# Kernel tuning notes

Hardware: AMD Instinct MI355X
Metric: run time of the kernel (lower is better)

The kernel has to match this reference:

```python
import jax, jax.numpy as jnp
import numpy as np

N_HEAD = 16

def setup_inputs() -> dict:
    key = jax.random.key(0)
    k1, k2, k3 = jax.random.split(key, 3)
    B, T, C = 2, 2048, 1024
    x_norm_for_qk = jax.random.normal(k1, (B, T, C), dtype=jnp.float32)
    xt_current_for_v = jax.random.normal(k2, (B, T, C), dtype=jnp.float32)
    W_attn = jax.random.normal(k3, (C, 2 * C), dtype=jnp.float32) * (1.0 / np.sqrt(C))
    b_attn = jnp.zeros((2 * C,), dtype=jnp.float32)
    return {"x_norm_for_qk": x_norm_for_qk, "xt_current_for_v": xt_current_for_v,
            "W_attn": W_attn, "b_attn": b_attn}

def reference(x_norm_for_qk, xt_current_for_v, W_attn, b_attn):
    B, T, C = x_norm_for_qk.shape
    H = N_HEAD
    D = C // H  # head dim
    qk = x_norm_for_qk @ W_attn + b_attn          # [B,T,2C]
    q, k = qk[..., :C], qk[..., C:]
    q = q.reshape(B, T, H, D).transpose(0, 2, 1, 3)   # [B,H,T,D]
    k = k.reshape(B, T, H, D).transpose(0, 2, 1, 3)
    v = xt_current_for_v.reshape(B, T, H, D).transpose(0, 2, 1, 3)
    scale = 1.0 / np.sqrt(D).astype(np.float32)
    scores = jnp.einsum('bhqd,bhkd->bhqk', q, k) * scale  # [B,H,T,T]
    causal = jnp.tril(jnp.ones((T, T), dtype=bool))
    scores = jnp.where(causal[None, None], scores, jnp.float32(-jnp.inf))
    weights = jax.nn.softmax(scores, axis=-1)  # dropout p=0.0 -> identity
    y = jnp.einsum('bhqk,bhkd->bhqd', weights, v)
    return y.transpose(0, 2, 1, 3).reshape(B, T, C)
```

## Files before the change

kernel.cpp:

```cpp
#include <hip/hip_runtime.h>
#include <hip/hip_bf16.h>
#include <math.h>

typedef __attribute__((ext_vector_type(8))) short s8v;
typedef __attribute__((ext_vector_type(4))) float f4v;
typedef __attribute__((ext_vector_type(16))) float f16v;
typedef __attribute__((ext_vector_type(2))) unsigned int u32x2;
typedef unsigned short ush;
typedef unsigned int u32;

#define QSCALE 0.180336880f
#define FIXED_M 10.0f

static __device__ __forceinline__ ush f2bf(float f) {
    u32 x = __builtin_bit_cast(u32, f);
    return (ush)((x + 0x7fffu + ((x >> 16) & 1u)) >> 16);
}
static __device__ __forceinline__ u32 bfpack(float lo, float hi) {
    u32 a = __builtin_bit_cast(u32, lo) + 0x8000u;
    u32 b = __builtin_bit_cast(u32, hi) + 0x8000u;
    return __builtin_amdgcn_perm(b, a, 0x07060302);
}
static __device__ __forceinline__ u32 cvtpk(float lo, float hi) {
    u32 r;
    asm("v_cvt_pk_bf16_f32 %0, %1, %2" : "=v"(r) : "v"(lo), "v"(hi));
    return r;
}
static __device__ __forceinline__ void gl_lds16(const void* g, void* l) {
    __builtin_amdgcn_global_load_lds(
        (const __attribute__((address_space(1))) u32*)g,
        (__attribute__((address_space(3))) u32*)l, 16, 0, 0);
}
#if __has_builtin(__builtin_amdgcn_exp2f)
#define EXP2F(x) __builtin_amdgcn_exp2f(x)
#else
#define EXP2F(x) exp2f(x)
#endif

static __device__ __forceinline__ void pl32swap(u32& a, u32& b) {
#if __has_builtin(__builtin_amdgcn_permlane32_swap)
    u32x2 r = __builtin_amdgcn_permlane32_swap(a, b, false, false);
    a = r[0]; b = r[1];
#else
    asm volatile("v_permlane32_swap_b32 %0, %1" : "+v"(a), "+v"(b));
#endif
}
static __device__ __forceinline__ s8v mkfrag(u32 a, u32 b, u32 c, u32 d) {
    union { u32 w[4]; s8v v; } u;
    u.w[0] = a; u.w[1] = b; u.w[2] = c; u.w[3] = d;
    return u.v;
}

static __device__ __forceinline__ void softpack32(
    const f16v& s0, bool needmask, int kbase, int qg,
    float& lrp, s8v& pfa, s8v& pfb)
{
    float ps = 0.f;
    u32 w0[4], w1[4];
    if (needmask) {
        #pragma unroll
        for (int g4 = 0; g4 < 4; ++g4) {
            const int kb0 = kbase + 8 * g4;
            float e0a = (kb0 + 0 > qg) ? 0.f : EXP2F(s0[g4 * 4 + 0] - FIXED_M);
            float e0b = (kb0 + 1 > qg) ? 0.f : EXP2F(s0[g4 * 4 + 1] - FIXED_M);
            float e0c = (kb0 + 2 > qg) ? 0.f : EXP2F(s0[g4 * 4 + 2] - FIXED_M);
            float e0d = (kb0 + 3 > qg) ? 0.f : EXP2F(s0[g4 * 4 + 3] - FIXED_M);
            ps += (e0a + e0b) + (e0c + e0d);
            w0[g4] = cvtpk(e0a, e0b); w1[g4] = cvtpk(e0c, e0d);
        }
    } else {
        #pragma unroll
        for (int g4 = 0; g4 < 4; ++g4) {
            float e0a = EXP2F(s0[g4 * 4 + 0] - FIXED_M);
            float e0b = EXP2F(s0[g4 * 4 + 1] - FIXED_M);
            float e0c = EXP2F(s0[g4 * 4 + 2] - FIXED_M);
            float e0d = EXP2F(s0[g4 * 4 + 3] - FIXED_M);
            ps += (e0a + e0b) + (e0c + e0d);
            w0[g4] = cvtpk(e0a, e0b); w1[g4] = cvtpk(e0c, e0d);
        }
    }
    lrp += ps;
    pl32swap(w0[0], w0[1]); pl32swap(w1[0], w1[1]);
    pl32swap(w0[2], w0[3]); pl32swap(w1[2], w1[3]);
    pfa = mkfrag(w0[0], w1[0], w0[1], w1[1]);
    pfb = mkfrag(w0[2], w1[2], w0[3], w1[3]);
}

__global__ __launch_bounds__(256) void prep_kernel(
    const float* __restrict__ X, const float* __restrict__ W,
    const float* __restrict__ XV,
    ush* __restrict__ Xb, ush* __restrict__ Wt, ush* __restrict__ Vtb)
{
    __shared__ float Ts[64][68];
    const int tid = threadIdx.x;
    const int bid = blockIdx.x;
    if (bid < 2048) {
        const size_t i = ((size_t)bid * 256 + tid) * 8;
        float4 v0 = *(const float4*)(X + i);
        float4 v1 = *(const float4*)(X + i + 4);
        uint4 o;
        o.x = bfpack(v0.x, v0.y); o.y = bfpack(v0.z, v0.w);
        o.z = bfpack(v1.x, v1.y); o.w = bfpack(v1.z, v1.w);
        *(uint4*)(Xb + i) = o;
    } else if (bid < 2560) {
        const int id = bid - 2048;
        const int n0 = (id & 31) * 64, k0 = (id >> 5) * 64;
        #pragma unroll
        for (int p = 0; p < 4; ++p) {
            const int idx = p * 256 + tid;
            const int kr = idx >> 4, nc4 = idx & 15;
            float4 v = *(const float4*)(W + (size_t)(k0 + kr) * 2048 + n0 + nc4 * 4);
            Ts[kr][nc4 * 4 + 0] = v.x; Ts[kr][nc4 * 4 + 1] = v.y;
            Ts[kr][nc4 * 4 + 2] = v.z; Ts[kr][nc4 * 4 + 3] = v.w;
        }
        __syncthreads();
        const int n = tid >> 2, kb = (tid & 3) * 16;
        #pragma unroll
        for (int p = 0; p < 4; ++p) {
            const int k = kb + p * 4;
            ushort4 o;
            o.x = f2bf(Ts[k + 0][n]); o.y = f2bf(Ts[k + 1][n]);
            o.z = f2bf(Ts[k + 2][n]); o.w = f2bf(Ts[k + 3][n]);
            *(ushort4*)(Wt + (size_t)(n0 + n) * 1024 + k0 + k) = o;
        }
    } else {
        const int id = bid - 2560;
        const int t0 = (id & 31) * 64;
        const int bh = id >> 5;
        const int b = bh >> 4, h = bh & 15;
        #pragma unroll
        for (int p = 0; p < 4; ++p) {
            const int idx = p * 256 + tid;
            const int tr = idx >> 4, dc4 = idx & 15;
            float4 v = *(const float4*)(XV + (size_t)(b * 2048 + t0 + tr) * 1024
                                        + h * 64 + dc4 * 4);
            Ts[tr][dc4 * 4 + 0] = v.x; Ts[tr][dc4 * 4 + 1] = v.y;
            Ts[tr][dc4 * 4 + 2] = v.z; Ts[tr][dc4 * 4 + 3] = v.w;
        }
        __syncthreads();
        const int d = tid >> 2, tb = (tid & 3) * 16;
        #pragma unroll
        for (int p = 0; p < 4; ++p) {
            const int tq = tb + p * 4;
            ushort4 o;
            o.x = f2bf(Ts[tq + 0][d]); o.y = f2bf(Ts[tq + 1][d]);
            o.z = f2bf(Ts[tq + 2][d]); o.w = f2bf(Ts[tq + 3][d]);
            *(ushort4*)(Vtb + (size_t)((b * 16 + h) * 64 + d) * 2048 + t0 + tq) = o;
        }
    }
}

__global__ __launch_bounds__(256, 2) void gemm_kernel(
    const ush* __restrict__ Xb, const ush* __restrict__ Wt,
    const float* __restrict__ bias,
    ush* __restrict__ Qb, ush* __restrict__ Kb)
{
    __shared__ ush As[4][128 * 32];
    __shared__ ush Bs[4][128 * 32];

    const int tid = threadIdx.x;
    const int wid = tid >> 6, lane = tid & 63;
    const int quad = lane >> 4, l15 = lane & 15;
    const int wm = wid >> 1, wn = wid & 1;
    const int m0 = blockIdx.y * 128, n0 = blockIdx.x * 128;

    const int lrow = lane >> 2;
    const int lkk = (lane & 3) * 8;
    const size_t arow = (size_t)(m0 + wid * 32 + lrow);
    const size_t brow = (size_t)(n0 + wid * 32 + lrow);

    auto stage = [&](int k) {
        const int k0 = k * 32, sl = k & 3;
        gl_lds16(Xb + arow * 1024 + k0 + lkk, &As[sl][wid * 1024]);
        gl_lds16(Xb + (arow + 16) * 1024 + k0 + lkk, &As[sl][wid * 1024 + 512]);
        gl_lds16(Wt + brow * 1024 + k0 + lkk, &Bs[sl][wid * 1024]);
        gl_lds16(Wt + (brow + 16) * 1024 + k0 + lkk, &Bs[sl][wid * 1024 + 512]);
    };

    f4v acc[4][4];
    #pragma unroll
    for (int i = 0; i < 4; ++i)
        #pragma unroll
        for (int j = 0; j < 4; ++j) acc[i][j] = (f4v){0.f, 0.f, 0.f, 0.f};

    stage(0); stage(1);
    asm volatile("s_waitcnt vmcnt(4)" ::: "memory");
    __builtin_amdgcn_s_barrier();
    __builtin_amdgcn_sched_barrier(0);

    for (int k = 0; k < 32; ++k) {
        const int sl = k & 3;
        const bool pf = (k + 2 < 32);

        s8v a[4], bf[4];
        #pragma unroll
        for (int i = 0; i < 4; ++i)
            a[i] = *(const s8v*)&As[sl][(wm * 64 + i * 16 + l15) * 32 + quad * 8];
        #pragma unroll
        for (int j = 0; j < 4; ++j)
            bf[j] = *(const s8v*)&Bs[sl][(wn * 64 + j * 16 + l15) * 32 + quad * 8];
        __builtin_amdgcn_sched_barrier(0);

        if (pf) stage(k + 2);

        __builtin_amdgcn_s_setprio(1);
        #pragma unroll
        for (int i = 0; i < 4; ++i)
            #pragma unroll
            for (int j = 0; j < 4; ++j)
                acc[i][j] = __builtin_amdgcn_mfma_f32_16x16x32_bf16(
                    a[i], bf[j], acc[i][j], 0, 0, 0);
        __builtin_amdgcn_s_setprio(0);

        if (pf) asm volatile("s_waitcnt vmcnt(4)" ::: "memory");
        else    asm volatile("s_waitcnt vmcnt(0)" ::: "memory");
        __builtin_amdgcn_s_barrier();
        __builtin_amdgcn_sched_barrier(0);
    }

    #pragma unroll
    for (int j = 0; j < 4; ++j) {
        const int n = n0 + wn * 64 + j * 16 + l15;
        const float bv = bias[n];
        const bool is_k = n >= 1024;
        const int nn = n & 1023;
        const int h = nn >> 6, d = nn & 63;
        ush* dst = is_k ? Kb : Qb;
        #pragma unroll
        for (int i = 0; i < 4; ++i) {
            const int mrow = m0 + wm * 64 + i * 16 + quad * 4;
            #pragma unroll
            for (int r = 0; r < 4; ++r) {
                const int m = mrow + r;
                const int b = m >> 11, t = m & 2047;
                float val = acc[i][j][r] + bv;
                if (!is_k) val *= QSCALE;
                dst[(size_t)((b * 16 + h) * 2048 + t) * 64 + d] = f2bf(val);
            }
        }
    }
}

__global__ __launch_bounds__(256, 2) void attn_kernel(
    const ush* __restrict__ Qb, const ush* __restrict__ Kb,
    const ush* __restrict__ Vt, float* __restrict__ Y)
{
    __shared__ ush SMEM[32768];
    ush* Kbuf = SMEM;
    ush* Vbuf = SMEM + 16384;

    const int tid = threadIdx.x;
    const int w = tid >> 6, lane = tid & 63;
    const int l31 = lane & 31, hi = lane >> 5;
    const int qh = w >> 1, kh = w & 1;

    const int idx = blockIdx.x;
    const int half = idx >> 8, pair = idx & 255;
    const int qt = half ? (pair & 15) : 15 - (pair & 15);
    const int bh = (pair >> 4) + half * 16;
    const int b = bh >> 4, h = bh & 15;
    const int q0 = qt * 128;
    const int ktmax = 2 * qt + 1;

    const ush* Qg = Qb + (size_t)bh * 2048 * 64;
    const ush* Kg = Kb + (size_t)bh * 2048 * 64;
    const ush* Vg = Vt + (size_t)bh * 64 * 2048;

    ush* Pw = SMEM + w * 2304;
    {
        const int r8q = lane >> 3, c8 = lane & 7;
        #pragma unroll
        for (int p = 0; p < 4; ++p) {
            const int row = p * 8 + r8q;
            uint4 v = *(const uint4*)(Qg + (size_t)(q0 + w * 32 + row) * 64 + c8 * 8);
            *(uint4*)&Pw[row * 72 + c8 * 8] = v;
        }
    }
    __syncthreads();
    s8v bq0[4], bq1[4];
    {
        const ush* P0 = SMEM + (qh * 2 + 0) * 2304 + l31 * 72;
        const ush* P1 = SMEM + (qh * 2 + 1) * 2304 + l31 * 72;
        #pragma unroll
        for (int s = 0; s < 4; ++s) {
            bq0[s] = *(const s8v*)&P0[s * 16 + hi * 8];
            bq1[s] = *(const s8v*)&P1[s * 16 + hi * 8];
        }
    }
    __syncthreads();

    const int r8 = lane >> 3;
    const int g8 = ((lane & 7) ^ r8) * 8;
    auto stage = [&](int kt) {
        const int buf = kt & 3;
        const int k0e = kt * 64;
        const ush* kg = Kg + (size_t)(k0e + w * 16 + r8) * 64 + g8;
        gl_lds16(kg, &Kbuf[buf * 4096 + (w * 16) * 64]);
        gl_lds16(kg + 8 * 64, &Kbuf[buf * 4096 + (w * 16 + 8) * 64]);
        const ush* vg = Vg + (size_t)(w * 16 + r8) * 2048 + k0e + g8;
        gl_lds16(vg, &Vbuf[buf * 4096 + (w * 16) * 64]);
        gl_lds16(vg + 8 * 2048, &Vbuf[buf * 4096 + (w * 16 + 8) * 64]);
    };

    f16v a00 = {}, a01 = {}, a10 = {}, a11 = {};
    float lrp0 = 0.f, lrp1 = 0.f;
    const int qbase = q0 + qh * 64;
    const int qg0 = qbase + l31;
    const int qg1 = qbase + 32 + l31;

    stage(0); stage(1);
    asm volatile("s_waitcnt vmcnt(4)" ::: "memory");
    __builtin_amdgcn_s_barrier();
    __builtin_amdgcn_sched_barrier(0);

    for (int kt = 0; kt <= ktmax; ++kt) {
        const int sl = (kt & 3) * 4096;
        const int keysmin = kt * 64 + kh * 32;
        const bool act0 = keysmin <= qbase + 31;
        const bool act1 = keysmin <= qbase + 63;
        const bool pf = (kt + 2 <= ktmax);

        s8v ak[4], av0[2], av1[2];
        if (act1) {
            const int krow = kh * 32 + l31;
            #pragma unroll
            for (int s = 0; s < 4; ++s) {
                const int ch = (s << 1) + hi;
                ak[s] = *(const s8v*)&Kbuf[sl + krow * 64 + ((ch ^ (krow & 7)) << 3)];
            }
            const int r0 = l31, r1 = 32 + l31;
            #pragma unroll
            for (int s = 0; s < 2; ++s) {
                const int ch = kh * 4 + (s << 1) + hi;
                av0[s] = *(const s8v*)&Vbuf[sl + r0 * 64 + ((ch ^ (r0 & 7)) << 3)];
                av1[s] = *(const s8v*)&Vbuf[sl + r1 * 64 + ((ch ^ (r1 & 7)) << 3)];
            }
        }
        __builtin_amdgcn_sched_barrier(0);

        if (pf) stage(kt + 2);

        if (act1) {
            const int kbase = keysmin + 4 * hi;
            const bool mask0 = (keysmin + 31) > qbase;
            const bool mask1 = (keysmin + 31) > (qbase + 32);

            if (act0) {
                f16v s0 = {};
                #pragma unroll
                for (int s = 0; s < 4; ++s)
                    s0 = __builtin_amdgcn_mfma_f32_32x32x16_bf16(ak[s], bq0[s], s0, 0, 0, 0);
                s8v pfa, pfb;
                softpack32(s0, mask0, kbase, qg0, lrp0, pfa, pfb);
                a00 = __builtin_amdgcn_mfma_f32_32x32x16_bf16(av0[0], pfa, a00, 0, 0, 0);
                a01 = __builtin_amdgcn_mfma_f32_32x32x16_bf16(av1[0], pfa, a01, 0, 0, 0);
                a00 = __builtin_amdgcn_mfma_f32_32x32x16_bf16(av0[1], pfb, a00, 0, 0, 0);
                a01 = __builtin_amdgcn_mfma_f32_32x32x16_bf16(av1[1], pfb, a01, 0, 0, 0);
            }
            {
                f16v s1 = {};
                #pragma unroll
                for (int s = 0; s < 4; ++s)
                    s1 = __builtin_amdgcn_mfma_f32_32x32x16_bf16(ak[s], bq1[s], s1, 0, 0, 0);
                s8v pfa, pfb;
                softpack32(s1, mask1, kbase, qg1, lrp1, pfa, pfb);
                a10 = __builtin_amdgcn_mfma_f32_32x32x16_bf16(av0[0], pfa, a10, 0, 0, 0);
                a11 = __builtin_amdgcn_mfma_f32_32x32x16_bf16(av1[0], pfa, a11, 0, 0, 0);
                a10 = __builtin_amdgcn_mfma_f32_32x32x16_bf16(av0[1], pfb, a10, 0, 0, 0);
                a11 = __builtin_amdgcn_mfma_f32_32x32x16_bf16(av1[1], pfb, a11, 0, 0, 0);
            }
        }

        if (pf) asm volatile("s_waitcnt vmcnt(4)" ::: "memory");
        else    asm volatile("s_waitcnt vmcnt(0)" ::: "memory");
        __builtin_amdgcn_s_barrier();
        __builtin_amdgcn_sched_barrier(0);
    }

    const float lq0 = lrp0 + __shfl_xor(lrp0, 32);
    const float lq1 = lrp1 + __shfl_xor(lrp1, 32);
    float* LTq = (float*)SMEM + qh * (64 * 68);
    float* Lx = (float*)SMEM + 2 * (64 * 68);

    if (kh == 1) {
        #pragma unroll
        for (int r = 0; r < 16; ++r) {
            const int d = (r & 3) + 8 * (r >> 2) + 4 * hi;
            LTq[l31 * 68 + d] = a00[r];
            LTq[l31 * 68 + 32 + d] = a01[r];
            LTq[(32 + l31) * 68 + d] = a10[r];
            LTq[(32 + l31) * 68 + 32 + d] = a11[r];
        }
        if (hi == 0) {
            Lx[qh * 64 + l31] = lq0;
            Lx[qh * 64 + 32 + l31] = lq1;
        }
    }
    __syncthreads();
    if (kh == 0) {
        const float li0 = 1.0f / (lq0 + Lx[qh * 64 + l31]);
        const float li1 = 1.0f / (lq1 + Lx[qh * 64 + 32 + l31]);
        #pragma unroll
        for (int r = 0; r < 16; ++r) {
            const int d = (r & 3) + 8 * (r >> 2) + 4 * hi;
            LTq[l31 * 68 + d] = (a00[r] + LTq[l31 * 68 + d]) * li0;
            LTq[l31 * 68 + 32 + d] = (a01[r] + LTq[l31 * 68 + 32 + d]) * li0;
            LTq[(32 + l31) * 68 + d] = (a10[r] + LTq[(32 + l31) * 68 + d]) * li1;
            LTq[(32 + l31) * 68 + 32 + d] = (a11[r] + LTq[(32 + l31) * 68 + 32 + d]) * li1;
        }
    }
    __syncthreads();
    const int qr4 = lane >> 4, chk = lane & 15;
    #pragma unroll
    for (int p = 0; p < 8; ++p) {
        const int qrow = w * 32 + p * 4 + qr4;
        const float* LTs = (float*)SMEM + (qrow >> 6) * (64 * 68);
        f4v v = *(const f4v*)&LTs[(qrow & 63) * 68 + chk * 4];
        *(float4*)(Y + (size_t)(b * 2048 + q0 + qrow) * 1024
                   + h * 64 + chk * 4) = (float4){v[0], v[1], v[2], v[3]};
    }
}

extern "C" void kernel_launch(void* const* d_in, const int* in_sizes, int n_in,
                              void* d_out, int out_size, void* d_ws,
                              size_t ws_size, hipStream_t stream)
{
    const float* x_qk = (const float*)d_in[0];
    const float* x_v  = (const float*)d_in[1];
    const float* W    = (const float*)d_in[2];
    const float* bias = (const float*)d_in[3];
    float* out = (float*)d_out;

    unsigned char* ws = (unsigned char*)d_ws;
    ush* Xb = (ush*)(ws);
    ush* Wt = (ush*)(ws + (8u << 20));
    ush* Qb = (ush*)(ws + (12u << 20));
    ush* Kb = (ush*)(ws + (20u << 20));
    ush* Vt = (ush*)(ws + (28u << 20));

    prep_kernel<<<3584, 256, 0, stream>>>(x_qk, W, x_v, Xb, Wt, Vt);
    gemm_kernel<<<dim3(16, 32), 256, 0, stream>>>(Xb, Wt, bias, Qb, Kb);
    attn_kernel<<<512, 256, 0, stream>>>(Qb, Kb, Vt, out);
}
```

Before: 143.3 us.

## Swizzle GEMM LDS tiles and stage epilogue through LDS for vectorized stores

The QK projection GEMM now XOR-swizzles the k-chunk position within each LDS row, on both the global-to-LDS staging and the MFMA fragment reads, to cut LDS bank conflicts. The epilogue first writes the biased, scaled bf16 tile into shared memory with a padded stride. It then reads it back as 16-byte vectors and writes contiguous head-dim rows to Q/K, replacing scattered 2-byte global stores. This adds a barrier and LDS traffic, and the two A/B buffers are merged into one flat array so the staging tile can reuse it.

```diff
diff --git a/kernel.cpp b/kernel.cpp
--- a/kernel.cpp
+++ b/kernel.cpp
@@ -155,8 +155,9 @@
     const float* __restrict__ bias,
     ush* __restrict__ Qb, ush* __restrict__ Kb)
 {
-    __shared__ ush As[4][128 * 32];
-    __shared__ ush Bs[4][128 * 32];
+    __shared__ ush SMEMG[32768];
+    ush* As = SMEMG;
+    ush* Bs = SMEMG + 16384;
 
     const int tid = threadIdx.x;
     const int wid = tid >> 6, lane = tid & 63;
@@ -165,16 +166,16 @@
     const int m0 = blockIdx.y * 128, n0 = blockIdx.x * 128;
 
     const int lrow = lane >> 2;
-    const int lkk = (lane & 3) * 8;
+    const int lkk = ((lane & 3) ^ (lrow & 3)) * 8;
     const size_t arow = (size_t)(m0 + wid * 32 + lrow);
     const size_t brow = (size_t)(n0 + wid * 32 + lrow);
 
     auto stage = [&](int k) {
         const int k0 = k * 32, sl = k & 3;
-        gl_lds16(Xb + arow * 1024 + k0 + lkk, &As[sl][wid * 1024]);
-        gl_lds16(Xb + (arow + 16) * 1024 + k0 + lkk, &As[sl][wid * 1024 + 512]);
-        gl_lds16(Wt + brow * 1024 + k0 + lkk, &Bs[sl][wid * 1024]);
-        gl_lds16(Wt + (brow + 16) * 1024 + k0 + lkk, &Bs[sl][wid * 1024 + 512]);
+        gl_lds16(Xb + arow * 1024 + k0 + lkk, &As[sl * 4096 + wid * 1024]);
+        gl_lds16(Xb + (arow + 16) * 1024 + k0 + lkk, &As[sl * 4096 + wid * 1024 + 512]);
+        gl_lds16(Wt + brow * 1024 + k0 + lkk, &Bs[sl * 4096 + wid * 1024]);
+        gl_lds16(Wt + (brow + 16) * 1024 + k0 + lkk, &Bs[sl * 4096 + wid * 1024 + 512]);
     };
 
     f4v acc[4][4];
@@ -188,6 +189,7 @@
     __builtin_amdgcn_s_barrier();
     __builtin_amdgcn_sched_barrier(0);
 
+    const int swc = (quad ^ (l15 & 3)) * 8;
     for (int k = 0; k < 32; ++k) {
         const int sl = k & 3;
         const bool pf = (k + 2 < 32);
@@ -195,10 +197,10 @@
         s8v a[4], bf[4];
         #pragma unroll
         for (int i = 0; i < 4; ++i)
-            a[i] = *(const s8v*)&As[sl][(wm * 64 + i * 16 + l15) * 32 + quad * 8];
+            a[i] = *(const s8v*)&As[sl * 4096 + (wm * 64 + i * 16 + l15) * 32 + swc];
         #pragma unroll
         for (int j = 0; j < 4; ++j)
-            bf[j] = *(const s8v*)&Bs[sl][(wn * 64 + j * 16 + l15) * 32 + quad * 8];
+            bf[j] = *(const s8v*)&Bs[sl * 4096 + (wn * 64 + j * 16 + l15) * 32 + swc];
         __builtin_amdgcn_sched_barrier(0);
 
         if (pf) stage(k + 2);
@@ -218,25 +220,35 @@
         __builtin_amdgcn_sched_barrier(0);
     }
 
+    ush* Ct = SMEMG;
     #pragma unroll
     for (int j = 0; j < 4; ++j) {
         const int n = n0 + wn * 64 + j * 16 + l15;
         const float bv = bias[n];
-        const bool is_k = n >= 1024;
-        const int nn = n & 1023;
-        const int h = nn >> 6, d = nn & 63;
-        ush* dst = is_k ? Kb : Qb;
+        const float sc = (n >= 1024) ? 1.0f : QSCALE;
+        const int cl = wn * 64 + j * 16 + l15;
         #pragma unroll
         for (int i = 0; i < 4; ++i) {
-            const int mrow = m0 + wm * 64 + i * 16 + quad * 4;
+            const int mrow = wm * 64 + i * 16 + quad * 4;
             #pragma unroll
-            for (int r = 0; r < 4; ++r) {
-                const int m = mrow + r;
-                const int b = m >> 11, t = m & 2047;
-                float val = acc[i][j][r] + bv;
-                if (!is_k) val *= QSCALE;
-                dst[(size_t)((b * 16 + h) * 2048 + t) * 64 + d] = f2bf(val);
-            }
+            for (int r = 0; r < 4; ++r)
+                Ct[(mrow + r) * 132 + cl] = f2bf((acc[i][j][r] + bv) * sc);
+        }
+    }
+    __syncthreads();
+    {
+        const bool is_k = n0 >= 1024;
+        ush* dstb = is_k ? Kb : Qb;
+        const int nc = tid & 15;
+        const int ng = n0 + nc * 8;
+        const int h = (ng >> 6) & 15, d = ng & 63;
+        #pragma unroll
+        for (int k = 0; k < 8; ++k) {
+            const int row = (tid >> 4) + k * 16;
+            const int m = m0 + row;
+            const int b = m >> 11, t = m & 2047;
+            uint4 v = *(const uint4*)&Ct[row * 132 + nc * 8];
+            *(uint4*)&dstb[(size_t)((b * 16 + h) * 2048 + t) * 64 + d] = v;
         }
     }
 }
```

New measurement: 148.2 us. 1.03x slower.
